# Optimization experiments

Hardware: AMD Instinct MI355X
Metric: run time of the kernel (lower is better)

The kernel has to match this reference:

```python
import jax, jax.numpy as jnp
import numpy as np

N = 100000   # nodes
E = 800000   # edges
IN = 64      # in_channels
H = 128      # hidden_channels (Embedding_Dimension)
K = 9        # Num_TCN clusters
EPS = 1e-15


def setup_inputs() -> dict:
    key = jax.random.key(0)
    k0, k1, k2, k3, k4 = jax.random.split(key, 5)
    x = jax.random.normal(k0, (N, IN), jnp.float32)
    edge_index = jax.random.randint(k1, (2, E), 0, N, dtype=jnp.int32)
    batch = jnp.zeros((N,), jnp.int32)  # single graph
    W1 = jax.random.normal(k2, (IN, H), jnp.float32) / np.sqrt(IN)
    b1 = jnp.zeros((H,), jnp.float32)
    Wp = jax.random.normal(k3, (H, K), jnp.float32) / np.sqrt(H)
    bp = jax.random.normal(k4, (K,), jnp.float32) * 0.01
    return {"x": x, "edge_index": edge_index, "batch": batch,
            "W1": W1, "b1": b1, "Wp": Wp, "bp": bp}


def gcn_conv(x, edge_index, W, b):
    # GCNConv: h = D^{-1/2} (A + I) D^{-1/2} (x W) + b
    n = x.shape[0]
    h = x @ W  # [N, H]
    loop = jnp.arange(n, dtype=edge_index.dtype)
    row = jnp.concatenate([edge_index[0], loop])  # source
    col = jnp.concatenate([edge_index[1], loop])  # target
    deg = jax.ops.segment_sum(jnp.ones_like(col, jnp.float32), col, n)
    dinv = jax.lax.rsqrt(jnp.maximum(deg, 1.0))  # deg >= 1 (self loops)
    norm = dinv[row] * dinv[col]  # [E+N]
    agg = jax.ops.segment_sum(norm[:, None] * h[row], col, n)  # scatter-add at targets
    return agg + b


def reference(x, edge_index, batch, W1, b1, Wp, bp):
    n = x.shape[0]
    src, dst = edge_index[0], edge_index[1]

    hx = jax.nn.relu(gcn_conv(x, edge_index, W1, b1))  # [N, H]
    s_logits = hx @ Wp + bp                             # [N, K]
    s = jax.nn.softmax(s_logits, axis=-1)

    # pooled features and adjacency: S^T X, S^T A S (A sparse via edge list)
    x_pool = s.T @ hx                                   # [K, H]
    out_adj = jnp.einsum('ek,el->kl', s[src], s[dst])   # [K, K]

    # mincut loss: -Tr(S^T A S) / Tr(S^T D S)
    mincut_num = jnp.trace(out_adj)
    deg_a = jax.ops.segment_sum(jnp.ones((src.shape[0],), jnp.float32), dst, n)
    mincut_den = jnp.sum(deg_a * jnp.sum(s * s, axis=-1))
    mc = -(mincut_num / (mincut_den + EPS))

    # orthogonality loss: || S^T S / ||S^T S||_F - I/sqrt(K) ||_F
    ss = s.T @ s
    o = jnp.linalg.norm(ss / jnp.linalg.norm(ss) - jnp.eye(K, dtype=s.dtype) / jnp.sqrt(jnp.float32(K)))

    # normalize pooled adjacency: zero diag, symmetric degree normalization
    oa = out_adj * (1.0 - jnp.eye(K, dtype=out_adj.dtype))
    d = jnp.sum(oa, axis=-1)
    dis = jax.lax.rsqrt(d + EPS)
    oa = dis[:, None] * oa * dis[None, :]

    out = jax.nn.log_softmax(x_pool[None], axis=-1)     # [1, K, H]
    return out, mc, o, s, oa[None]
```

## Files before the change

kernel.cpp:

```cpp
#include <hip/hip_runtime.h>
#include <hip/hip_bf16.h>

#define NN 100000
#define NE 800000
#define INC 64
#define HID 128
#define KC 9
#define NBKT 782
#define BCAP 2048
#define LDA 72
#define LDH 132

#define G_XP 0
#define G_OA 1152
#define G_SS 1233
#define G_DEN 1314

typedef __attribute__((ext_vector_type(8))) short bfrag;
typedef __attribute__((ext_vector_type(4))) float facc4;

__device__ __forceinline__ float atomAddG(float* p, float v) {
  return unsafeAtomicAdd(p, v);
}

__device__ __forceinline__ unsigned short bf16rn(float x) {
  unsigned u = __float_as_uint(x);
  return (unsigned short)((u + 0x7fffu + ((u >> 16) & 1u)) >> 16);
}


__global__ __launch_bounds__(256) void k_binA(const int* __restrict__ src, const int* __restrict__ dst,
                                              const float* __restrict__ W1, const float* __restrict__ Wp,
                                              int* __restrict__ bcur, int* __restrict__ ebuf,
                                              unsigned short* __restrict__ W1Thi,
                                              unsigned short* __restrict__ W1Tlo,
                                              float* __restrict__ wpsT) {
  int t = threadIdx.x;
  if (blockIdx.x == 128) {
    for (int i = t; i < (INC * HID) / 4; i += 256) {
      int k = i >> 5, c4 = (i & 31) * 4;
      float4 v = ((const float4*)W1)[i];
      float vv[4] = {v.x, v.y, v.z, v.w};
#pragma unroll
      for (int j = 0; j < 4; ++j) {
        unsigned short h = bf16rn(vv[j]);
        float lo = vv[j] - __uint_as_float((unsigned)h << 16);
        W1Thi[(c4 + j) * 64 + k] = h;
        W1Tlo[(c4 + j) * 64 + k] = bf16rn(lo);
      }
    }
    for (int i = t; i < KC * HID; i += 256) {
      int q = i >> 7, c = i & 127;
      wpsT[i] = Wp[c * KC + q];
    }
    return;
  }
  __shared__ int hist[NBKT];
  __shared__ int hbase[NBKT];
  for (int b = t; b < NBKT; b += 256) hist[b] = 0;
  __syncthreads();
  int beg = blockIdx.x * 6250, end = beg + 6250;
  for (int i = beg + t; i < end; i += 256) atomicAdd(&hist[dst[i] >> 7], 1);
  __syncthreads();
  for (int b = t; b < NBKT; b += 256) {
    int h = hist[b];
    hbase[b] = h ? atomicAdd(&bcur[b], h) : 0;
    hist[b] = 0;
  }
  __syncthreads();
  for (int i = beg + t; i < end; i += 256) {
    int d = dst[i], s = src[i];
    int b = d >> 7;
    int r = atomicAdd(&hist[b], 1);
    ebuf[(size_t)b * BCAP + hbase[b] + r] = s | ((d & 127) << 17);
  }
}

__global__ __launch_bounds__(256) void k_scanb(const int* __restrict__ bcur, int* __restrict__ bbase) {
  __shared__ int sc[1024];
  int t = threadIdx.x;
  for (int i = t; i < 1024; i += 256) sc[i] = (i < NBKT) ? bcur[i] : 0;
  __syncthreads();
  for (int off = 1; off < 1024; off <<= 1) {
    int v0 = (t >= off) ? sc[t - off] : 0;
    int v1 = (t + 256 >= off) ? sc[t + 256 - off] : 0;
    int v2 = (t + 512 >= off) ? sc[t + 512 - off] : 0;
    int v3 = (t + 768 >= off) ? sc[t + 768 - off] : 0;
    __syncthreads();
    sc[t] += v0; sc[t + 256] += v1; sc[t + 512] += v2; sc[t + 768] += v3;
    __syncthreads();
  }
  for (int i = t; i < NBKT; i += 256) bbase[i] = sc[i] - bcur[i];
}

__global__ __launch_bounds__(256) void k_fillB(const int* __restrict__ bcur, const int* __restrict__ bbase,
                                               const int* __restrict__ ebuf, int* __restrict__ rowptr,
                                               int* __restrict__ degi, float* __restrict__ dinv,
                                               int* __restrict__ csr) {
  __shared__ int cnt[128], loc[128], lcur[128];
  int b = blockIdx.x;
  int t = threadIdx.x;
  if (t < 128) cnt[t] = 0;
  __syncthreads();
  int n = bcur[b];
  const int* eb = ebuf + (size_t)b * BCAP;
  for (int i = t; i < n; i += 256) atomicAdd(&cnt[eb[i] >> 17], 1);
  __syncthreads();
  if (t < 128) loc[t] = cnt[t];
  __syncthreads();
  for (int off = 1; off < 128; off <<= 1) {
    int u = (t >= off && t < 128) ? loc[t - off] : 0;
    __syncthreads();
    if (t < 128) loc[t] += u;
    __syncthreads();
  }
  int gbase = bbase[b];
  if (t < 128) {
    int node = (b << 7) + t;
    int rp = gbase + loc[t] - cnt[t];
    if (node < NN) {
      rowptr[node] = rp;
      degi[node] = cnt[t];
      dinv[node] = rsqrtf((float)cnt[t] + 1.f);
    }
    lcur[t] = rp;
  }
  __syncthreads();
  for (int i = t; i < n; i += 256) {
    int pack = eb[i];
    int s = pack & 0x1FFFF;
    int dl = pack >> 17;
    int p = atomicAdd(&lcur[dl], 1);
    csr[p] = s;
  }
}


__global__ __launch_bounds__(256) void k_gather(const int* __restrict__ rowptr, const int* __restrict__ degi,
                                                const int* __restrict__ csr, const float* __restrict__ x,
                                                const float* __restrict__ dinv, float* __restrict__ agg) {
  int t = threadIdx.x;
  int wave = t >> 6, lane = t & 63;
  int gw = blockIdx.x * 4 + wave;
  int ng = lane >> 4, c4 = lane & 15;
  int node = gw * 4 + ng;
  if (node >= NN) return;

  float dv = dinv[node];
  int base = rowptr[node];
  int cnt = degi[node];

  float4 xs = ((const float4*)(x + (size_t)node * INC))[c4];
  float dv2 = dv * dv;
  float4 acc;
  acc.x = dv2 * xs.x; acc.y = dv2 * xs.y; acc.z = dv2 * xs.z; acc.w = dv2 * xs.w;

  int j = 0;
  for (; j + 3 < cnt; j += 4) {
    int s0 = csr[base + j], s1 = csr[base + j + 1], s2 = csr[base + j + 2], s3 = csr[base + j + 3];
    float w0 = dinv[s0] * dv, w1 = dinv[s1] * dv, w2 = dinv[s2] * dv, w3 = dinv[s3] * dv;
    float4 r0 = ((const float4*)(x + (size_t)s0 * INC))[c4];
    float4 r1 = ((const float4*)(x + (size_t)s1 * INC))[c4];
    float4 r2 = ((const float4*)(x + (size_t)s2 * INC))[c4];
    float4 r3 = ((const float4*)(x + (size_t)s3 * INC))[c4];
    acc.x = fmaf(w0, r0.x, acc.x); acc.y = fmaf(w0, r0.y, acc.y);
    acc.z = fmaf(w0, r0.z, acc.z); acc.w = fmaf(w0, r0.w, acc.w);
    acc.x = fmaf(w1, r1.x, acc.x); acc.y = fmaf(w1, r1.y, acc.y);
    acc.z = fmaf(w1, r1.z, acc.z); acc.w = fmaf(w1, r1.w, acc.w);
    acc.x = fmaf(w2, r2.x, acc.x); acc.y = fmaf(w2, r2.y, acc.y);
    acc.z = fmaf(w2, r2.z, acc.z); acc.w = fmaf(w2, r2.w, acc.w);
    acc.x = fmaf(w3, r3.x, acc.x); acc.y = fmaf(w3, r3.y, acc.y);
    acc.z = fmaf(w3, r3.z, acc.z); acc.w = fmaf(w3, r3.w, acc.w);
  }
  for (; j < cnt; ++j) {
    int si = csr[base + j];
    float w = dinv[si] * dv;
    float4 r = ((const float4*)(x + (size_t)si * INC))[c4];
    acc.x = fmaf(w, r.x, acc.x); acc.y = fmaf(w, r.y, acc.y);
    acc.z = fmaf(w, r.z, acc.z); acc.w = fmaf(w, r.w, acc.w);
  }
  ((float4*)(agg + (size_t)node * INC))[c4] = acc;
}


__global__ __launch_bounds__(256, 2) void k_mlpA(const float* __restrict__ agg,
                                                 const unsigned short* __restrict__ W1Thi,
                                                 const unsigned short* __restrict__ W1Tlo,
                                                 const float* __restrict__ wpsT_g,
                                                 const float* __restrict__ b1, const float* __restrict__ bp,
                                                 float* __restrict__ s_out, float* __restrict__ s_pad,
                                                 float* __restrict__ pool_part) {
  __shared__ char smem[78336];
  short* Ahi = (short*)smem;
  short* Alo = Ahi + 128 * LDA;
  short* Whi = Alo + 128 * LDA;
  short* Wlo = Whi + 128 * LDA;
  float* Hs = (float*)smem;
  float* s_lds = Hs + 128 * LDH;
  float* wpsT = (float*)(smem + 73728);

  int t = threadIdx.x;
  int nbase = blockIdx.x * 128;

#pragma unroll
  for (int j = 0; j < 8; ++j) {
    int task = t + 256 * j;
    int n = task >> 4, kq = (task & 15) * 4;
    float4 v = make_float4(0.f, 0.f, 0.f, 0.f);
    if (nbase + n < NN) v = *(const float4*)(agg + (size_t)(nbase + n) * INC + kq);
    unsigned short h0 = bf16rn(v.x), h1 = bf16rn(v.y), h2 = bf16rn(v.z), h3 = bf16rn(v.w);
    float l0f = v.x - __uint_as_float((unsigned)h0 << 16);
    float l1f = v.y - __uint_as_float((unsigned)h1 << 16);
    float l2f = v.z - __uint_as_float((unsigned)h2 << 16);
    float l3f = v.w - __uint_as_float((unsigned)h3 << 16);
    unsigned short q0 = bf16rn(l0f), q1 = bf16rn(l1f), q2 = bf16rn(l2f), q3 = bf16rn(l3f);
    *(uint2*)&Ahi[n * LDA + kq] = make_uint2((unsigned)h0 | ((unsigned)h1 << 16),
                                             (unsigned)h2 | ((unsigned)h3 << 16));
    *(uint2*)&Alo[n * LDA + kq] = make_uint2((unsigned)q0 | ((unsigned)q1 << 16),
                                             (unsigned)q2 | ((unsigned)q3 << 16));
  }
#pragma unroll
  for (int j = 0; j < 8; ++j) {
    int task = t + 256 * j;
    int c = task >> 4, k4 = (task & 15) * 4;
    *(uint2*)&Whi[c * LDA + k4] = *(const uint2*)&W1Thi[c * 64 + k4];
    *(uint2*)&Wlo[c * LDA + k4] = *(const uint2*)&W1Tlo[c * 64 + k4];
  }
  for (int i = t; i < KC * HID; i += 256) wpsT[i] = wpsT_g[i];
  __syncthreads();

  int w = t >> 6, l = t & 63;
  int r0 = w * 32;
  int lrow = l & 15;
  int lk = (l >> 4) * 8;
  int rg = (l >> 4) * 4;

  facc4 acc[2][8];
#pragma unroll
  for (int mt = 0; mt < 2; ++mt)
#pragma unroll
    for (int nt = 0; nt < 8; ++nt) acc[mt][nt] = (facc4){0.f, 0.f, 0.f, 0.f};

#pragma unroll
  for (int ks = 0; ks < 2; ++ks) {
    int ko = ks * 32 + lk;
    bfrag a0h = *(const bfrag*)&Ahi[(r0 + lrow) * LDA + ko];
    bfrag a0l = *(const bfrag*)&Alo[(r0 + lrow) * LDA + ko];
    bfrag a1h = *(const bfrag*)&Ahi[(r0 + 16 + lrow) * LDA + ko];
    bfrag a1l = *(const bfrag*)&Alo[(r0 + 16 + lrow) * LDA + ko];
#pragma unroll
    for (int nt = 0; nt < 8; ++nt) {
      bfrag bh = *(const bfrag*)&Whi[(nt * 16 + lrow) * LDA + ko];
      bfrag bl = *(const bfrag*)&Wlo[(nt * 16 + lrow) * LDA + ko];
      acc[0][nt] = __builtin_amdgcn_mfma_f32_16x16x32_bf16(a0l, bh, acc[0][nt], 0, 0, 0);
      acc[0][nt] = __builtin_amdgcn_mfma_f32_16x16x32_bf16(a0h, bl, acc[0][nt], 0, 0, 0);
      acc[0][nt] = __builtin_amdgcn_mfma_f32_16x16x32_bf16(a0h, bh, acc[0][nt], 0, 0, 0);
      acc[1][nt] = __builtin_amdgcn_mfma_f32_16x16x32_bf16(a1l, bh, acc[1][nt], 0, 0, 0);
      acc[1][nt] = __builtin_amdgcn_mfma_f32_16x16x32_bf16(a1h, bl, acc[1][nt], 0, 0, 0);
      acc[1][nt] = __builtin_amdgcn_mfma_f32_16x16x32_bf16(a1h, bh, acc[1][nt], 0, 0, 0);
    }
  }
  __syncthreads();

#pragma unroll
  for (int nt = 0; nt < 8; ++nt) {
    float b1v = b1[nt * 16 + lrow];
#pragma unroll
    for (int mt = 0; mt < 2; ++mt)
#pragma unroll
      for (int r = 0; r < 4; ++r)
        Hs[(r0 + mt * 16 + rg + r) * LDH + nt * 16 + lrow] =
            fmaxf(acc[mt][nt][r] + b1v, 0.f);
  }
  __syncthreads();

  {
    int node = t >> 1, half = t & 1;
    const float4* hrow = (const float4*)(Hs + node * LDH + half * 64);
    float4 h4[16];
#pragma unroll
    for (int cc = 0; cc < 16; ++cc) h4[cc] = hrow[cc];

    float lg[KC];
#pragma unroll
    for (int q = 0; q < KC; ++q) {
      const float4* w4 = (const float4*)(wpsT + q * HID + half * 64);
      float s0 = 0.f, s1 = 0.f, s2 = 0.f, s3 = 0.f;
#pragma unroll
      for (int cc = 0; cc < 16; ++cc) {
        float4 wv = w4[cc];
        s0 = fmaf(h4[cc].x, wv.x, s0);
        s1 = fmaf(h4[cc].y, wv.y, s1);
        s2 = fmaf(h4[cc].z, wv.z, s2);
        s3 = fmaf(h4[cc].w, wv.w, s3);
      }
      lg[q] = (s0 + s1) + (s2 + s3);
    }
#pragma unroll
    for (int q = 0; q < KC; ++q)
      lg[q] = lg[q] + __shfl_xor(lg[q], 1, 64) + bp[q];

    float m = lg[0];
#pragma unroll
    for (int q = 1; q < KC; ++q) m = fmaxf(m, lg[q]);
    float Z = 0.f;
#pragma unroll
    for (int q = 0; q < KC; ++q) { lg[q] = __expf(lg[q] - m); Z += lg[q]; }
    float inv = 1.0f / Z;
#pragma unroll
    for (int q = 0; q < KC; ++q) lg[q] *= inv;

    float4* sl = (float4*)(s_lds + node * 12);
    int gnode = nbase + node;
    if (half == 0) {
      sl[0] = make_float4(lg[0], lg[1], lg[2], lg[3]);
      if (gnode < NN) {
        ((float4*)(s_pad + (size_t)gnode * 12))[0] = make_float4(lg[0], lg[1], lg[2], lg[3]);
        float* so = s_out + (size_t)gnode * KC;
        so[0] = lg[0]; so[1] = lg[1]; so[2] = lg[2]; so[3] = lg[3]; so[4] = lg[4];
      }
    } else {
      sl[1] = make_float4(lg[4], lg[5], lg[6], lg[7]);
      s_lds[node * 12 + 8] = lg[8];
      if (gnode < NN) {
        ((float4*)(s_pad + (size_t)gnode * 12))[1] = make_float4(lg[4], lg[5], lg[6], lg[7]);
        ((float4*)(s_pad + (size_t)gnode * 12))[2] = make_float4(lg[8], 0.f, 0.f, 0.f);
        float* so = s_out + (size_t)gnode * KC;
        so[5] = lg[5]; so[6] = lg[6]; so[7] = lg[7]; so[8] = lg[8];
      }
    }
  }
  __syncthreads();

  {
    int c = t & 127, nh = t >> 7;
    float pool[KC];
#pragma unroll
    for (int q = 0; q < KC; ++q) pool[q] = 0.f;
    int lim = NN - nbase - nh * 64;
    if (lim > 64) lim = 64;
    for (int i = 0; i < lim; ++i) {
      int node = nh * 64 + i;
      float4 sa = *(const float4*)(s_lds + node * 12);
      float4 sb = *(const float4*)(s_lds + node * 12 + 4);
      float s8 = s_lds[node * 12 + 8];
      float h = Hs[node * LDH + c];
      pool[0] = fmaf(sa.x, h, pool[0]);
      pool[1] = fmaf(sa.y, h, pool[1]);
      pool[2] = fmaf(sa.z, h, pool[2]);
      pool[3] = fmaf(sa.w, h, pool[3]);
      pool[4] = fmaf(sb.x, h, pool[4]);
      pool[5] = fmaf(sb.y, h, pool[5]);
      pool[6] = fmaf(sb.z, h, pool[6]);
      pool[7] = fmaf(sb.w, h, pool[7]);
      pool[8] = fmaf(s8, h, pool[8]);
    }
    float* pp = pool_part + (size_t)(blockIdx.x * 2 + nh) * (KC * HID);
#pragma unroll
    for (int q = 0; q < KC; ++q) pp[q * HID + c] = pool[q];
  }
}


__global__ __launch_bounds__(256) void k_ssden(const float* __restrict__ s_pad,
                                               const int* __restrict__ degi,
                                               const float* __restrict__ pool_part,
                                               float* __restrict__ glob) {
  int t = threadIdx.x;
  int tid = blockIdx.x * 256 + t;
  int stride = gridDim.x * 256;

  {
    float a0 = 0.f, a1 = 0.f, a2 = 0.f, a3 = 0.f, a4 = 0.f;
    for (int p = blockIdx.x; p < 2 * NBKT; p += gridDim.x) {
      const float* row = pool_part + (size_t)p * (KC * HID);
      a0 += row[t];
      a1 += row[t + 256];
      a2 += row[t + 512];
      a3 += row[t + 768];
      if (t < 128) a4 += row[t + 1024];
    }
    atomAddG(&glob[G_XP + t], a0);
    atomAddG(&glob[G_XP + t + 256], a1);
    atomAddG(&glob[G_XP + t + 512], a2);
    atomAddG(&glob[G_XP + t + 768], a3);
    if (t < 128) atomAddG(&glob[G_XP + t + 1024], a4);
  }

  float acc[81];
  float den = 0.f;
#pragma unroll
  for (int i = 0; i < 81; ++i) acc[i] = 0.f;

  for (int node = tid; node < NN; node += stride) {
    const float4* sn = (const float4*)(s_pad + (size_t)node * 12);
    float4 a = sn[0], b = sn[1], c = sn[2];
    float s[9] = {a.x, a.y, a.z, a.w, b.x, b.y, b.z, b.w, c.x};
    float dg = (float)degi[node];
    float nrm = 0.f;
#pragma unroll
    for (int i = 0; i < 9; ++i) nrm = fmaf(s[i], s[i], nrm);
    den = fmaf(dg, nrm, den);
#pragma unroll
    for (int i = 0; i < 9; ++i)
#pragma unroll
      for (int j = 0; j < 9; ++j) acc[i * 9 + j] = fmaf(s[i], s[j], acc[i * 9 + j]);
  }

  __shared__ float wsum[4][82];
#pragma unroll
  for (int i = 0; i < 81; ++i) {
#pragma unroll
    for (int off = 32; off > 0; off >>= 1) acc[i] += __shfl_xor(acc[i], off, 64);
  }
#pragma unroll
  for (int off = 32; off > 0; off >>= 1) den += __shfl_xor(den, off, 64);
  int wave = t >> 6, lane = t & 63;
  if (lane == 0) {
#pragma unroll
    for (int i = 0; i < 81; ++i) wsum[wave][i] = acc[i];
    wsum[wave][81] = den;
  }
  __syncthreads();
  if (t < 81) atomAddG(&glob[G_SS + t], wsum[0][t] + wsum[1][t] + wsum[2][t] + wsum[3][t]);
  if (t == 81) atomAddG(&glob[G_DEN], wsum[0][81] + wsum[1][81] + wsum[2][81] + wsum[3][81]);
}


__global__ __launch_bounds__(256) void k_adj(const int* __restrict__ rowptr, const int* __restrict__ degi,
                                             const int* __restrict__ csr, const float* __restrict__ s_pad,
                                             float* __restrict__ oa_g) {
  int t = threadIdx.x;
  int tid = blockIdx.x * blockDim.x + t;
  int stride = gridDim.x * blockDim.x;

  float acc[81];
#pragma unroll
  for (int i = 0; i < 81; ++i) acc[i] = 0.f;

  for (int node = tid; node < NN; node += stride) {
    int base = rowptr[node];
    int cnt = degi[node];
    float4 g0 = make_float4(0.f, 0.f, 0.f, 0.f);
    float4 g1 = g0;
    float g8 = 0.f;
    int j = 0;
    for (; j + 1 < cnt; j += 2) {
      int s0 = csr[base + j], s1 = csr[base + j + 1];
      const float4* p0 = (const float4*)(s_pad + (size_t)s0 * 12);
      const float4* p1 = (const float4*)(s_pad + (size_t)s1 * 12);
      float4 a0 = p0[0], b0 = p0[1], c0 = p0[2];
      float4 a1 = p1[0], b1 = p1[1], c1 = p1[2];
      g0.x += a0.x + a1.x; g0.y += a0.y + a1.y; g0.z += a0.z + a1.z; g0.w += a0.w + a1.w;
      g1.x += b0.x + b1.x; g1.y += b0.y + b1.y; g1.z += b0.z + b1.z; g1.w += b0.w + b1.w;
      g8 += c0.x + c1.x;
    }
    if (j < cnt) {
      int s0 = csr[base + j];
      const float4* p0 = (const float4*)(s_pad + (size_t)s0 * 12);
      float4 a0 = p0[0], b0 = p0[1], c0 = p0[2];
      g0.x += a0.x; g0.y += a0.y; g0.z += a0.z; g0.w += a0.w;
      g1.x += b0.x; g1.y += b0.y; g1.z += b0.z; g1.w += b0.w;
      g8 += c0.x;
    }
    const float4* sn = (const float4*)(s_pad + (size_t)node * 12);
    float4 d0 = sn[0], d1 = sn[1], d2 = sn[2];
    float gg[9] = {g0.x, g0.y, g0.z, g0.w, g1.x, g1.y, g1.z, g1.w, g8};
    float sd[9] = {d0.x, d0.y, d0.z, d0.w, d1.x, d1.y, d1.z, d1.w, d2.x};
#pragma unroll
    for (int i = 0; i < 9; ++i)
#pragma unroll
      for (int jj = 0; jj < 9; ++jj) acc[i * 9 + jj] = fmaf(gg[i], sd[jj], acc[i * 9 + jj]);
  }

  __shared__ float wsum[4][81];
#pragma unroll
  for (int i = 0; i < 81; ++i) {
#pragma unroll
    for (int off = 32; off > 0; off >>= 1) acc[i] += __shfl_xor(acc[i], off, 64);
  }
  int wave = t >> 6, lane = t & 63;
  if (lane == 0) {
#pragma unroll
    for (int i = 0; i < 81; ++i) wsum[wave][i] = acc[i];
  }
  __syncthreads();
  if (t < 81) atomAddG(&oa_g[t], wsum[0][t] + wsum[1][t] + wsum[2][t] + wsum[3][t]);
}


__global__ __launch_bounds__(128) void k_final(const float* __restrict__ glob, float* __restrict__ out) {
  const float* xp = glob + G_XP;
  const float* oa = glob + G_OA;
  const float* ssm = glob + G_SS;
  const float* den = glob + G_DEN;
  int t = threadIdx.x;
  __shared__ float red[128];

  for (int k = 0; k < 9; ++k) {
    float v = xp[k * 128 + t];
    red[t] = v;
    __syncthreads();
    for (int s2 = 64; s2 > 0; s2 >>= 1) {
      if (t < s2) red[t] = fmaxf(red[t], red[t + s2]);
      __syncthreads();
    }
    float m = red[0];
    __syncthreads();
    red[t] = expf(v - m);
    __syncthreads();
    for (int s2 = 64; s2 > 0; s2 >>= 1) {
      if (t < s2) red[t] += red[t + s2];
      __syncthreads();
    }
    float lz = logf(red[0]) + m;
    __syncthreads();
    out[k * 128 + t] = v - lz;
  }

  if (t == 0) {
    float num = 0.f;
    for (int q = 0; q < 9; ++q) num += oa[q * 9 + q];
    out[1152] = -(num / (den[0] + 1e-15f));

    float fn = 0.f;
    for (int i = 0; i < 81; ++i) fn += ssm[i] * ssm[i];
    float rfn = 1.0f / sqrtf(fn);
    float osum = 0.f;
    for (int i = 0; i < 9; ++i)
      for (int j = 0; j < 9; ++j) {
        float v = ssm[i * 9 + j] * rfn - ((i == j) ? (1.0f / 3.0f) : 0.f);
        osum += v * v;
      }
    out[1153] = sqrtf(osum);
  }

  __shared__ float dsh[9];
  if (t < 9) {
    float d = 0.f;
    for (int j = 0; j < 9; ++j)
      if (j != t) d += oa[t * 9 + j];
    dsh[t] = 1.0f / sqrtf(d + 1e-15f);
  }
  __syncthreads();
  if (t < 81) {
    int i = t / 9, j = t % 9;
    out[901154 + t] = (i == j) ? 0.f : dsh[i] * oa[t] * dsh[j];
  }
}

extern "C" void kernel_launch(void* const* d_in, const int* in_sizes, int n_in,
                              void* d_out, int out_size, void* d_ws, size_t ws_size,
                              hipStream_t stream) {
  const float* x = (const float*)d_in[0];
  const int* ei = (const int*)d_in[1];
  const float* W1 = (const float*)d_in[3];
  const float* b1 = (const float*)d_in[4];
  const float* Wp = (const float*)d_in[5];
  const float* bp = (const float*)d_in[6];
  float* out = (float*)d_out;

  float* glob = (float*)d_ws;
  int* bcur = (int*)d_ws + 1316;
  int* bbase = (int*)d_ws + 2116;
  int* rowptr = (int*)d_ws + 2944;
  int* degi = rowptr + NN;
  int* csr = degi + NN;
  float* dinv = (float*)(csr + NE);
  float* s_pad = dinv + NN;
  float* agg = s_pad + (size_t)NN * 12;
  int* ebuf = (int*)(agg + (size_t)NN * INC);
  float* pool_part = (float*)(ebuf + (size_t)NBKT * BCAP);
  unsigned short* W1Thi = (unsigned short*)(pool_part + (size_t)NBKT * 2 * (KC * HID));
  unsigned short* W1Tlo = W1Thi + INC * HID;
  float* wpsT = (float*)(W1Tlo + INC * HID);

  hipMemsetAsync(d_ws, 0, (size_t)2116 * sizeof(float), stream);

  const int* src = ei;
  const int* dst = ei + NE;

  hipLaunchKernelGGL(k_binA, dim3(129), dim3(256), 0, stream, src, dst, W1, Wp,
                     bcur, ebuf, W1Thi, W1Tlo, wpsT);
  hipLaunchKernelGGL(k_scanb, dim3(1), dim3(256), 0, stream, bcur, bbase);
  hipLaunchKernelGGL(k_fillB, dim3(NBKT), dim3(256), 0, stream, bcur, bbase, ebuf,
                     rowptr, degi, dinv, csr);
  hipLaunchKernelGGL(k_gather, dim3(6250), dim3(256), 0, stream, rowptr, degi, csr, x, dinv, agg);
  hipLaunchKernelGGL(k_mlpA, dim3(NBKT), dim3(256), 0, stream, agg,
                     W1Thi, W1Tlo, wpsT, b1, bp, out + 1154, s_pad, pool_part);
  hipLaunchKernelGGL(k_ssden, dim3(128), dim3(256), 0, stream, s_pad, degi, pool_part, glob);
  hipLaunchKernelGGL(k_adj, dim3(1024), dim3(256), 0, stream, rowptr, degi, csr, s_pad, glob + G_OA);
  hipLaunchKernelGGL(k_final, dim3(1), dim3(128), 0, stream, glob, out);
}
```

Measured before the change: 249.3 us.

## Fuse neighbor aggregation gather into MLP kernel, removing agg buffer

The separate gather kernel that computed normalized neighbor aggregation into a global agg buffer is removed. The aggregation now runs inside k_mlpA, which splits the result directly into hi/lo bf16 tiles in LDS. This drops one kernel launch and the write and re-read of a 100000x64 float intermediate. In exchange, the latency-bound gather now runs in only 782 blocks limited by the MLP kernel's LDS and launch bounds, so there is less parallelism to hide the irregular memory latency.

```diff
diff --git a/kernel.cpp b/kernel.cpp
--- a/kernel.cpp
+++ b/kernel.cpp
@@ -136,54 +136,11 @@
 }
 
 
-__global__ __launch_bounds__(256) void k_gather(const int* __restrict__ rowptr, const int* __restrict__ degi,
-                                                const int* __restrict__ csr, const float* __restrict__ x,
-                                                const float* __restrict__ dinv, float* __restrict__ agg) {
-  int t = threadIdx.x;
-  int wave = t >> 6, lane = t & 63;
-  int gw = blockIdx.x * 4 + wave;
-  int ng = lane >> 4, c4 = lane & 15;
-  int node = gw * 4 + ng;
-  if (node >= NN) return;
-
-  float dv = dinv[node];
-  int base = rowptr[node];
-  int cnt = degi[node];
-
-  float4 xs = ((const float4*)(x + (size_t)node * INC))[c4];
-  float dv2 = dv * dv;
-  float4 acc;
-  acc.x = dv2 * xs.x; acc.y = dv2 * xs.y; acc.z = dv2 * xs.z; acc.w = dv2 * xs.w;
-
-  int j = 0;
-  for (; j + 3 < cnt; j += 4) {
-    int s0 = csr[base + j], s1 = csr[base + j + 1], s2 = csr[base + j + 2], s3 = csr[base + j + 3];
-    float w0 = dinv[s0] * dv, w1 = dinv[s1] * dv, w2 = dinv[s2] * dv, w3 = dinv[s3] * dv;
-    float4 r0 = ((const float4*)(x + (size_t)s0 * INC))[c4];
-    float4 r1 = ((const float4*)(x + (size_t)s1 * INC))[c4];
-    float4 r2 = ((const float4*)(x + (size_t)s2 * INC))[c4];
-    float4 r3 = ((const float4*)(x + (size_t)s3 * INC))[c4];
-    acc.x = fmaf(w0, r0.x, acc.x); acc.y = fmaf(w0, r0.y, acc.y);
-    acc.z = fmaf(w0, r0.z, acc.z); acc.w = fmaf(w0, r0.w, acc.w);
-    acc.x = fmaf(w1, r1.x, acc.x); acc.y = fmaf(w1, r1.y, acc.y);
-    acc.z = fmaf(w1, r1.z, acc.z); acc.w = fmaf(w1, r1.w, acc.w);
-    acc.x = fmaf(w2, r2.x, acc.x); acc.y = fmaf(w2, r2.y, acc.y);
-    acc.z = fmaf(w2, r2.z, acc.z); acc.w = fmaf(w2, r2.w, acc.w);
-    acc.x = fmaf(w3, r3.x, acc.x); acc.y = fmaf(w3, r3.y, acc.y);
-    acc.z = fmaf(w3, r3.z, acc.z); acc.w = fmaf(w3, r3.w, acc.w);
-  }
-  for (; j < cnt; ++j) {
-    int si = csr[base + j];
-    float w = dinv[si] * dv;
-    float4 r = ((const float4*)(x + (size_t)si * INC))[c4];
-    acc.x = fmaf(w, r.x, acc.x); acc.y = fmaf(w, r.y, acc.y);
-    acc.z = fmaf(w, r.z, acc.z); acc.w = fmaf(w, r.w, acc.w);
-  }
-  ((float4*)(agg + (size_t)node * INC))[c4] = acc;
-}
-
-
-__global__ __launch_bounds__(256, 2) void k_mlpA(const float* __restrict__ agg,
+__global__ __launch_bounds__(256, 2) void k_mlpA(const float* __restrict__ x,
+                                                 const int* __restrict__ rowptr,
+                                                 const int* __restrict__ degi,
+                                                 const int* __restrict__ csr,
+                                                 const float* __restrict__ dinv,
                                                  const unsigned short* __restrict__ W1Thi,
                                                  const unsigned short* __restrict__ W1Tlo,
                                                  const float* __restrict__ wpsT_g,
@@ -205,28 +162,65 @@
 #pragma unroll
   for (int j = 0; j < 8; ++j) {
     int task = t + 256 * j;
-    int n = task >> 4, kq = (task & 15) * 4;
-    float4 v = make_float4(0.f, 0.f, 0.f, 0.f);
-    if (nbase + n < NN) v = *(const float4*)(agg + (size_t)(nbase + n) * INC + kq);
-    unsigned short h0 = bf16rn(v.x), h1 = bf16rn(v.y), h2 = bf16rn(v.z), h3 = bf16rn(v.w);
-    float l0f = v.x - __uint_as_float((unsigned)h0 << 16);
-    float l1f = v.y - __uint_as_float((unsigned)h1 << 16);
-    float l2f = v.z - __uint_as_float((unsigned)h2 << 16);
-    float l3f = v.w - __uint_as_float((unsigned)h3 << 16);
-    unsigned short q0 = bf16rn(l0f), q1 = bf16rn(l1f), q2 = bf16rn(l2f), q3 = bf16rn(l3f);
-    *(uint2*)&Ahi[n * LDA + kq] = make_uint2((unsigned)h0 | ((unsigned)h1 << 16),
-                                             (unsigned)h2 | ((unsigned)h3 << 16));
-    *(uint2*)&Alo[n * LDA + kq] = make_uint2((unsigned)q0 | ((unsigned)q1 << 16),
-                                             (unsigned)q2 | ((unsigned)q3 << 16));
-  }
-#pragma unroll
-  for (int j = 0; j < 8; ++j) {
-    int task = t + 256 * j;
     int c = task >> 4, k4 = (task & 15) * 4;
     *(uint2*)&Whi[c * LDA + k4] = *(const uint2*)&W1Thi[c * 64 + k4];
     *(uint2*)&Wlo[c * LDA + k4] = *(const uint2*)&W1Tlo[c * 64 + k4];
   }
   for (int i = t; i < KC * HID; i += 256) wpsT[i] = wpsT_g[i];
+
+  {
+    int g = t >> 4, c4 = t & 15;
+#pragma unroll 1
+    for (int rep = 0; rep < 8; ++rep) {
+      int nl = rep * 16 + g;
+      int gnode = nbase + nl;
+      float4 acc = make_float4(0.f, 0.f, 0.f, 0.f);
+      if (gnode < NN) {
+        float dv = dinv[gnode];
+        int base = rowptr[gnode];
+        int cnt = degi[gnode];
+        float4 xs = ((const float4*)(x + (size_t)gnode * INC))[c4];
+        float dv2 = dv * dv;
+        acc.x = dv2 * xs.x; acc.y = dv2 * xs.y; acc.z = dv2 * xs.z; acc.w = dv2 * xs.w;
+        int j = 0;
+        for (; j + 3 < cnt; j += 4) {
+          int s0 = csr[base + j], s1 = csr[base + j + 1];
+          int s2 = csr[base + j + 2], s3 = csr[base + j + 3];
+          float w0 = dinv[s0] * dv, w1 = dinv[s1] * dv, w2 = dinv[s2] * dv, w3 = dinv[s3] * dv;
+          float4 r0 = ((const float4*)(x + (size_t)s0 * INC))[c4];
+          float4 r1 = ((const float4*)(x + (size_t)s1 * INC))[c4];
+          float4 r2 = ((const float4*)(x + (size_t)s2 * INC))[c4];
+          float4 r3 = ((const float4*)(x + (size_t)s3 * INC))[c4];
+          acc.x = fmaf(w0, r0.x, acc.x); acc.y = fmaf(w0, r0.y, acc.y);
+          acc.z = fmaf(w0, r0.z, acc.z); acc.w = fmaf(w0, r0.w, acc.w);
+          acc.x = fmaf(w1, r1.x, acc.x); acc.y = fmaf(w1, r1.y, acc.y);
+          acc.z = fmaf(w1, r1.z, acc.z); acc.w = fmaf(w1, r1.w, acc.w);
+          acc.x = fmaf(w2, r2.x, acc.x); acc.y = fmaf(w2, r2.y, acc.y);
+          acc.z = fmaf(w2, r2.z, acc.z); acc.w = fmaf(w2, r2.w, acc.w);
+          acc.x = fmaf(w3, r3.x, acc.x); acc.y = fmaf(w3, r3.y, acc.y);
+          acc.z = fmaf(w3, r3.z, acc.z); acc.w = fmaf(w3, r3.w, acc.w);
+        }
+        for (; j < cnt; ++j) {
+          int si = csr[base + j];
+          float w = dinv[si] * dv;
+          float4 r = ((const float4*)(x + (size_t)si * INC))[c4];
+          acc.x = fmaf(w, r.x, acc.x); acc.y = fmaf(w, r.y, acc.y);
+          acc.z = fmaf(w, r.z, acc.z); acc.w = fmaf(w, r.w, acc.w);
+        }
+      }
+      unsigned short h0 = bf16rn(acc.x), h1 = bf16rn(acc.y);
+      unsigned short h2 = bf16rn(acc.z), h3 = bf16rn(acc.w);
+      float l0f = acc.x - __uint_as_float((unsigned)h0 << 16);
+      float l1f = acc.y - __uint_as_float((unsigned)h1 << 16);
+      float l2f = acc.z - __uint_as_float((unsigned)h2 << 16);
+      float l3f = acc.w - __uint_as_float((unsigned)h3 << 16);
+      unsigned short q0 = bf16rn(l0f), q1 = bf16rn(l1f), q2 = bf16rn(l2f), q3 = bf16rn(l3f);
+      *(uint2*)&Ahi[nl * LDA + c4 * 4] = make_uint2((unsigned)h0 | ((unsigned)h1 << 16),
+                                                    (unsigned)h2 | ((unsigned)h3 << 16));
+      *(uint2*)&Alo[nl * LDA + c4 * 4] = make_uint2((unsigned)q0 | ((unsigned)q1 << 16),
+                                                    (unsigned)q2 | ((unsigned)q3 << 16));
+    }
+  }
   __syncthreads();
 
   int w = t >> 6, l = t & 63;
@@ -568,8 +562,7 @@
   int* csr = degi + NN;
   float* dinv = (float*)(csr + NE);
   float* s_pad = dinv + NN;
-  float* agg = s_pad + (size_t)NN * 12;
-  int* ebuf = (int*)(agg + (size_t)NN * INC);
+  int* ebuf = (int*)(s_pad + (size_t)NN * 12);
   float* pool_part = (float*)(ebuf + (size_t)NBKT * BCAP);
   unsigned short* W1Thi = (unsigned short*)(pool_part + (size_t)NBKT * 2 * (KC * HID));
   unsigned short* W1Tlo = W1Thi + INC * HID;
@@ -585,8 +578,7 @@
   hipLaunchKernelGGL(k_scanb, dim3(1), dim3(256), 0, stream, bcur, bbase);
   hipLaunchKernelGGL(k_fillB, dim3(NBKT), dim3(256), 0, stream, bcur, bbase, ebuf,
                      rowptr, degi, dinv, csr);
-  hipLaunchKernelGGL(k_gather, dim3(6250), dim3(256), 0, stream, rowptr, degi, csr, x, dinv, agg);
-  hipLaunchKernelGGL(k_mlpA, dim3(NBKT), dim3(256), 0, stream, agg,
+  hipLaunchKernelGGL(k_mlpA, dim3(NBKT), dim3(256), 0, stream, x, rowptr, degi, csr, dinv,
                      W1Thi, W1Tlo, wpsT, b1, bp, out + 1154, s_pad, pool_part);
   hipLaunchKernelGGL(k_ssden, dim3(128), dim3(256), 0, stream, s_pad, degi, pool_part, glob);
   hipLaunchKernelGGL(k_adj, dim3(1024), dim3(256), 0, stream, rowptr, degi, csr, s_pad, glob + G_OA);
```

Measured after the change: 272.8 us. 1.09x slower.
